# Kernel tuning notes

Measured on AMD Instinct MI355X. Metric: run time of the kernel, lower is better.

The kernel has to match this reference:

```python
import jax, jax.numpy as jnp
import numpy as np

N, F_IN, HID, H1, NG = 50000, 128, 64, 4, 512
E = 800000


def setup_inputs() -> dict:
    key = jax.random.key(0)
    ks = jax.random.split(key, 16)
    x = jax.random.normal(ks[0], (N, F_IN), dtype=jnp.float32)
    edge_index = jax.random.randint(ks[1], (2, E), 0, N, dtype=jnp.int64)
    batch = jnp.sort(jax.random.randint(ks[2], (N,), 0, NG, dtype=jnp.int64))
    s = 0.05
    W1 = jax.random.normal(ks[3], (F_IN, H1 * HID), dtype=jnp.float32) * s
    a_src1 = jax.random.normal(ks[4], (H1, HID), dtype=jnp.float32) * s
    a_dst1 = jax.random.normal(ks[5], (H1, HID), dtype=jnp.float32) * s
    b1 = jnp.zeros((H1 * HID,), dtype=jnp.float32)
    W2 = jax.random.normal(ks[6], (H1 * HID, HID), dtype=jnp.float32) * s
    a_src2 = jax.random.normal(ks[7], (1, HID), dtype=jnp.float32) * s
    a_dst2 = jax.random.normal(ks[8], (1, HID), dtype=jnp.float32) * s
    b2 = jnp.zeros((HID,), dtype=jnp.float32)
    Wc = jax.random.normal(ks[9], (HID, 2), dtype=jnp.float32) * s
    bc = jnp.zeros((2,), dtype=jnp.float32)
    return dict(x=x, edge_index=edge_index, batch=batch, W1=W1, a_src1=a_src1,
                a_dst1=a_dst1, b1=b1, W2=W2, a_src2=a_src2, a_dst2=a_dst2,
                b2=b2, Wc=Wc, bc=bc)


def gat_layer(x, W, a_src, a_dst, bias, src, dst, n):
    # PyG GATConv: h = x @ W per head; e_ij = LeakyReLU(a_src.h_j + a_dst.h_i),
    # softmax over incoming edges of each dst node, then scatter-add aggregate.
    H, D = a_src.shape
    h = (x @ W).reshape(n, H, D)                       # [N,H,D]
    asrc = jnp.einsum('nhd,hd->nh', h, a_src)          # [N,H]
    adst = jnp.einsum('nhd,hd->nh', h, a_dst)
    e = jax.nn.leaky_relu(asrc[src] + adst[dst], 0.2)  # [E,H]
    m = jax.lax.stop_gradient(jax.ops.segment_max(e, dst, num_segments=n))
    p = jnp.exp(e - m[dst])
    s = jax.ops.segment_sum(p, dst, num_segments=n)
    alpha = p / (s[dst] + 1e-16)                       # [E,H]
    out = jax.ops.segment_sum(alpha[:, :, None] * h[src], dst, num_segments=n)
    return out.reshape(n, H * D) + bias


def reference(x, edge_index, batch, W1, a_src1, a_dst1, b1, W2, a_src2, a_dst2, b2, Wc, bc):
    n = x.shape[0]
    loops = jnp.arange(n, dtype=edge_index.dtype)
    src = jnp.concatenate([edge_index[0], loops])  # add self-loops (PyG default)
    dst = jnp.concatenate([edge_index[1], loops])
    h = jax.nn.relu(gat_layer(x, W1, a_src1, a_dst1, b1, src, dst, n))
    h = jax.nn.relu(gat_layer(h, W2, a_src2, a_dst2, b2, src, dst, n))
    # global mean pool over graphs
    ng = NG
    sums = jax.ops.segment_sum(h, batch, num_segments=ng)
    cnts = jax.ops.segment_sum(jnp.ones((n,), h.dtype), batch, num_segments=ng)
    pooled = sums / jnp.maximum(cnts, 1.0)[:, None]
    logits = pooled @ Wc + bc
    return jax.nn.log_softmax(logits, axis=1)
```

## Files before the change

kernel.cpp:

```cpp
#include <hip/hip_runtime.h>
#include <hip/hip_bf16.h>
#include <cstddef>
#include <cstdint>

#define FIN   128
#define HID   64
#define H1    4
#define NGRAPH 512
#define BCAP  8192
#define PREB  512

typedef short bf16x8 __attribute__((ext_vector_type(8)));
typedef float f32x4  __attribute__((ext_vector_type(4)));

#if defined(__has_builtin)
#if __has_builtin(__builtin_amdgcn_cvt_f32_fp8) && __has_builtin(__builtin_amdgcn_cvt_pk_fp8_f32)
#define HAVE_HW_FP8 1
#endif
#endif

__device__ __forceinline__ float wave_reduce_sum(float v) {
  #pragma unroll
  for (int off = 32; off > 0; off >>= 1) v += __shfl_down(v, off, 64);
  return v;
}

__device__ __forceinline__ float leaky02(float x) {
  return x > 0.0f ? x : 0.2f * x;
}

__device__ __forceinline__ unsigned short f2bf(float f) {
  union { float f; unsigned int i; } v; v.f = f;
  unsigned int b = v.i;
  return (unsigned short)((b + 0x7FFFu + ((b >> 16) & 1u)) >> 16);
}

#ifndef HAVE_HW_FP8
__device__ __forceinline__ unsigned char f2fp8_1(float f) {
  unsigned int u = __float_as_uint(f);
  unsigned int s = u >> 31;
  u &= 0x7fffffffu;
  if (u > 0x43e00000u) u = 0x43e00000u;
  unsigned int b = u + (0x0007FFFFu + ((u >> 20) & 1u));
  int e = (int)(b >> 23) - 127;
  unsigned int m = (b >> 20) & 7u;
  unsigned char o;
  if (e < -9) o = 0;
  else if (e < -6) { int sh = -6 - e; o = (unsigned char)((8u | m) >> sh); }
  else if (e > 8) o = 0x7e;
  else o = (unsigned char)(((e + 7) << 3) | m);
  return o | (unsigned char)(s << 7);
}
__device__ __forceinline__ float fp8tof_1(unsigned char b) {
  unsigned int s = b >> 7, e = (b >> 3) & 15u, m = b & 7u;
  float v = (e == 0) ? (float)m * 0.001953125f
                     : (float)(8u + m) * __uint_as_float((117u + e) << 23);
  return s ? -v : v;
}
#endif

__device__ __forceinline__ unsigned char f2fp8(float f) {
#ifdef HAVE_HW_FP8
  return (unsigned char)(__builtin_amdgcn_cvt_pk_fp8_f32(f, f, 0u, false) & 0xffu);
#else
  return f2fp8_1(f);
#endif
}
__device__ __forceinline__ float fp8dec(unsigned int w, int i) {
#ifdef HAVE_HW_FP8
  switch (i) {
    case 0: return __builtin_amdgcn_cvt_f32_fp8(w, 0);
    case 1: return __builtin_amdgcn_cvt_f32_fp8(w, 1);
    case 2: return __builtin_amdgcn_cvt_f32_fp8(w, 2);
    default: return __builtin_amdgcn_cvt_f32_fp8(w, 3);
  }
#else
  return fp8tof_1((unsigned char)((w >> (8 * i)) & 0xffu));
#endif
}

__global__ __launch_bounds__(256)
void pre_kernel(const float* __restrict__ W1, const float* __restrict__ W2,
                unsigned short* __restrict__ W1T, unsigned short* __restrict__ W2T,
                const int* __restrict__ dst, int* __restrict__ bucketCnt,
                const int* __restrict__ batch, int* __restrict__ gstart,
                int* __restrict__ gend, int E, int N, int nbuck) {
  __shared__ int lh[256];
  int tid = threadIdx.x;
  lh[tid] = 0;
  __syncthreads();
  int stride = gridDim.x * 256;
  int t0 = blockIdx.x * 256 + tid;
  for (int i = t0; i < E; i += stride)
    atomicAdd(&lh[dst[i] >> 8], 1);
  for (int i = t0; i < N; i += stride) {
    int g = batch[i];
    if (i == 0 || batch[i - 1] != g) gstart[g] = i;
    if (i == N - 1 || batch[i + 1] != g) gend[g] = i + 1;
  }
  for (int u = t0; u < 256 * 128; u += stride) {
    int n = u >> 7, k = u & 127;
    W1T[u] = f2bf(W1[(size_t)k * 256 + n]);
  }
  for (int u = t0; u < 64 * 256; u += stride) {
    int n = u >> 8, k = u & 255;
    W2T[u] = f2bf(W2[(size_t)k * 64 + n]);
  }
  __syncthreads();
  if (tid < nbuck && lh[tid] > 0) atomicAdd(&bucketCnt[tid], lh[tid]);
}

#define P3K 16
__global__ __launch_bounds__(256)
void bpart_kernel(const int* __restrict__ src, const int* __restrict__ dst,
                  int* __restrict__ bucketFill, unsigned int* __restrict__ bucketBuf,
                  int E, int nbuck) {
  __shared__ int lhist[256];
  __shared__ int lbase[256];
  int tid = threadIdx.x;
  int chunk = 256 * P3K;
  for (int start = blockIdx.x * chunk; start < E; start += gridDim.x * chunk) {
    lhist[tid] = 0;
    __syncthreads();
    int mybuck[P3K]; unsigned int mypack[P3K]; int myrank[P3K];
    #pragma unroll
    for (int k = 0; k < P3K; k++) {
      int i = start + k * 256 + tid;
      if (i < E) {
        int d = dst[i];
        int b = d >> 8;
        mybuck[k] = b;
        mypack[k] = (unsigned int)src[i] | ((unsigned int)(d & 255) << 16);
        myrank[k] = atomicAdd(&lhist[b], 1);
      } else mybuck[k] = -1;
    }
    __syncthreads();
    if (tid < nbuck) lbase[tid] = (lhist[tid] > 0) ? atomicAdd(&bucketFill[tid], lhist[tid]) : 0;
    __syncthreads();
    #pragma unroll
    for (int k = 0; k < P3K; k++) {
      if (mybuck[k] >= 0) {
        int b = mybuck[k];
        int pos = lbase[b] + myrank[k];
        if (pos < BCAP) bucketBuf[((size_t)b << 13) + pos] = mypack[k];
      }
    }
    __syncthreads();
  }
}

__global__ __launch_bounds__(256)
void bbuild_kernel(const unsigned int* __restrict__ bucketBuf, const int* __restrict__ bucketCnt,
                   int* __restrict__ rowstart, int* __restrict__ rowend,
                   unsigned short* __restrict__ csr, int N) {
  __shared__ int ldeg[256];
  __shared__ int lscan[256];
  __shared__ int lfill[256];
  int b = blockIdx.x;
  int tid = threadIdx.x;
  int r0 = b << 13;
  int cnt = bucketCnt[b]; if (cnt > BCAP) cnt = BCAP;
  int nb0 = b << 8;
  ldeg[tid] = 0;
  __syncthreads();
  for (int j = tid; j < cnt; j += 256)
    atomicAdd(&ldeg[bucketBuf[r0 + j] >> 16], 1);
  __syncthreads();
  int v = ldeg[tid];
  lscan[tid] = v;
  __syncthreads();
  for (int off = 1; off < 256; off <<= 1) {
    int u = (tid >= off) ? lscan[tid - off] : 0;
    __syncthreads();
    lscan[tid] += u;
    __syncthreads();
  }
  int excl = lscan[tid] - v;
  lfill[tid] = excl;
  if (nb0 + tid < N) {
    rowstart[nb0 + tid] = r0 + excl;
    rowend[nb0 + tid]   = r0 + excl + v;
  }
  __syncthreads();
  for (int j = tid; j < cnt; j += 256) {
    unsigned int p = bucketBuf[r0 + j];
    int pos = r0 + atomicAdd(&lfill[p >> 16], 1);
    csr[pos] = (unsigned short)(p & 0xffffu);
  }
}

__global__ __launch_bounds__(256)
void gemm1_kernel(const float* __restrict__ X, const unsigned short* __restrict__ W1T,
                  unsigned char* __restrict__ h1f8,
                  const float* __restrict__ a_src, const float* __restrict__ a_dst,
                  float* __restrict__ asv, float* __restrict__ adv, int N) {
  __shared__ unsigned short As[64][136];
  __shared__ unsigned short Bs[256][40];
  int t = threadIdx.x;
  int w = t >> 6, lane = t & 63;
  int quad = lane >> 4, l16 = lane & 15;
  int blockRow = blockIdx.x * 64;

  {
    int node = t >> 2, kp = (t & 3) * 32;
    int gn = blockRow + node; if (gn >= N) gn = N - 1;
    const float4* xp = (const float4*)(X + (size_t)gn * 128 + kp);
    #pragma unroll
    for (int i = 0; i < 4; i++) {
      float4 va = xp[2 * i], vb = xp[2 * i + 1];
      union { unsigned short u[8]; uint4 v; } r;
      r.u[0] = f2bf(va.x); r.u[1] = f2bf(va.y); r.u[2] = f2bf(va.z); r.u[3] = f2bf(va.w);
      r.u[4] = f2bf(vb.x); r.u[5] = f2bf(vb.y); r.u[6] = f2bf(vb.z); r.u[7] = f2bf(vb.w);
      *(uint4*)&As[node][kp + i * 8] = r.v;
    }
  }

  f32x4 acc[4][4];
  #pragma unroll
  for (int i = 0; i < 4; i++)
    #pragma unroll
    for (int j = 0; j < 4; j++) acc[i][j] = (f32x4){0.f, 0.f, 0.f, 0.f};

  for (int kc = 0; kc < FIN; kc += 32) {
    {
      const unsigned short* wp = W1T + (size_t)t * 128 + kc;
      #pragma unroll
      for (int i = 0; i < 4; i++) {
        uint4 v = *(const uint4*)(wp + i * 8);
        *(uint4*)&Bs[t][i * 8] = v;
      }
    }
    __syncthreads();
    bf16x8 af[4], bfr[4];
    #pragma unroll
    for (int mt = 0; mt < 4; mt++)
      af[mt] = *(const bf16x8*)&As[mt * 16 + l16][kc + quad * 8];
    #pragma unroll
    for (int nt = 0; nt < 4; nt++)
      bfr[nt] = *(const bf16x8*)&Bs[w * 64 + nt * 16 + l16][quad * 8];
    #pragma unroll
    for (int mt = 0; mt < 4; mt++)
      #pragma unroll
      for (int nt = 0; nt < 4; nt++)
        acc[mt][nt] = __builtin_amdgcn_mfma_f32_16x16x32_bf16(af[mt], bfr[nt], acc[mt][nt], 0, 0, 0);
    __syncthreads();
  }

  float a_s[4], a_d[4];
  #pragma unroll
  for (int nt = 0; nt < 4; nt++) {
    a_s[nt] = a_src[w * 64 + nt * 16 + l16];
    a_d[nt] = a_dst[w * 64 + nt * 16 + l16];
  }
  #pragma unroll
  for (int mt = 0; mt < 4; mt++) {
    #pragma unroll
    for (int reg = 0; reg < 4; reg++) {
      int node = blockRow + mt * 16 + quad * 4 + reg;
      bool ok = node < N;
      float ps = 0.0f, pd = 0.0f;
      #pragma unroll
      for (int nt = 0; nt < 4; nt++) {
        float v = acc[mt][nt][reg];
        ps = fmaf(v, a_s[nt], ps);
        pd = fmaf(v, a_d[nt], pd);
        if (ok) h1f8[(size_t)node * 256 + w * 64 + nt * 16 + l16] = f2fp8(v);
      }
      #pragma unroll
      for (int off = 8; off > 0; off >>= 1) {
        ps += __shfl_xor(ps, off, 16);
        pd += __shfl_xor(pd, off, 16);
      }
      if (l16 == 0 && ok) {
        asv[(size_t)node * 4 + w] = ps;
        adv[(size_t)node * 4 + w] = pd;
      }
    }
  }
}

__global__ __launch_bounds__(256)
void gemm2_kernel(const unsigned short* __restrict__ out1b, const unsigned short* __restrict__ W2T,
                  unsigned char* __restrict__ h2f8,
                  const float* __restrict__ a_src, const float* __restrict__ a_dst,
                  float* __restrict__ asv, float* __restrict__ adv, int N) {
  __shared__ unsigned short As[64][40];
  __shared__ unsigned short Bs[64][40];
  int t = threadIdx.x;
  int w = t >> 6, lane = t & 63;
  int quad = lane >> 4, l16 = lane & 15;
  int blockRow = blockIdx.x * 64;

  f32x4 acc[4];
  #pragma unroll
  for (int j = 0; j < 4; j++) acc[j] = (f32x4){0.f, 0.f, 0.f, 0.f};

  int nodeS = t >> 2, koff = (t & 3) * 8;
  int gnS = blockRow + nodeS; if (gnS >= N) gnS = N - 1;

  for (int kc = 0; kc < 256; kc += 32) {
    {
      uint4 va = *(const uint4*)(out1b + (size_t)gnS * 256 + kc + koff);
      *(uint4*)&As[nodeS][koff] = va;
      uint4 vb = *(const uint4*)(W2T + (size_t)nodeS * 256 + kc + koff);
      *(uint4*)&Bs[nodeS][koff] = vb;
    }
    __syncthreads();
    bf16x8 af = *(const bf16x8*)&As[w * 16 + l16][quad * 8];
    #pragma unroll
    for (int nt = 0; nt < 4; nt++) {
      bf16x8 bfr = *(const bf16x8*)&Bs[nt * 16 + l16][quad * 8];
      acc[nt] = __builtin_amdgcn_mfma_f32_16x16x32_bf16(af, bfr, acc[nt], 0, 0, 0);
    }
    __syncthreads();
  }

  float a_s[4], a_d[4];
  #pragma unroll
  for (int nt = 0; nt < 4; nt++) {
    a_s[nt] = a_src[nt * 16 + l16];
    a_d[nt] = a_dst[nt * 16 + l16];
  }
  #pragma unroll
  for (int reg = 0; reg < 4; reg++) {
    int node = blockRow + w * 16 + quad * 4 + reg;
    bool ok = node < N;
    float ps = 0.0f, pd = 0.0f;
    #pragma unroll
    for (int nt = 0; nt < 4; nt++) {
      float v = acc[nt][reg];
      ps = fmaf(v, a_s[nt], ps);
      pd = fmaf(v, a_d[nt], pd);
      if (ok) h2f8[(size_t)node * 64 + nt * 16 + l16] = f2fp8(v);
    }
    #pragma unroll
    for (int off = 8; off > 0; off >>= 1) {
      ps += __shfl_xor(ps, off, 16);
      pd += __shfl_xor(pd, off, 16);
    }
    if (l16 == 0 && ok) { asv[node] = ps; adv[node] = pd; }
  }
}

__global__ __launch_bounds__(256)
void agg1_kernel(const unsigned char* __restrict__ h1f8, const int* __restrict__ rowstart,
                 const int* __restrict__ rowend, const unsigned short* __restrict__ csr,
                 const float* __restrict__ asv, const float* __restrict__ adv,
                 const float* __restrict__ b1, unsigned short* __restrict__ out1b, int N) {
  __shared__ int   sbuf[4][64];
  __shared__ float pbuf[4][4][68];
  int wv   = threadIdx.x >> 6;
  int lane = threadIdx.x & 63;
  int n = blockIdx.x * 4 + wv;
  if (n >= N) return;
  int r0 = rowstart[n], r1 = rowend[n];
  float4 ad = *(const float4*)(adv + (size_t)n * 4);
  float4 asn = *(const float4*)(asv + (size_t)n * 4);
  int hsel = lane >> 4;

  float es0 = leaky02(asn.x + ad.x);
  float es1 = leaky02(asn.y + ad.y);
  float es2 = leaky02(asn.z + ad.z);
  float es3 = leaky02(asn.w + ad.w);
  float esel = hsel == 0 ? es0 : (hsel == 1 ? es1 : (hsel == 2 ? es2 : es3));
  float m0r = es0, m1r = es1, m2r = es2, m3r = es3;
  float mselr = esel;
  float ssum = 0.0f;
  float a0 = 0, a1 = 0, a2 = 0, a3 = 0;

  for (int base = r0; base < r1; base += 64) {
    int j = base + lane;
    int cnt = min(64, r1 - base);
    float e0 = -1e30f, e1 = -1e30f, e2 = -1e30f, e3 = -1e30f;
    if (j < r1) {
      int s = csr[j];
      float4 as = *(const float4*)(asv + (size_t)s * 4);
      sbuf[wv][lane] = s;
      e0 = leaky02(as.x + ad.x);
      e1 = leaky02(as.y + ad.y);
      e2 = leaky02(as.z + ad.z);
      e3 = leaky02(as.w + ad.w);
    }
    float f0 = e0, f1 = e1, f2 = e2, f3 = e3;
    #pragma unroll
    for (int off = 32; off > 0; off >>= 1) {
      e0 = fmaxf(e0, __shfl_xor(e0, off, 64));
      e1 = fmaxf(e1, __shfl_xor(e1, off, 64));
      e2 = fmaxf(e2, __shfl_xor(e2, off, 64));
      e3 = fmaxf(e3, __shfl_xor(e3, off, 64));
    }
    float m0n = fmaxf(m0r, e0), m1n = fmaxf(m1r, e1);
    float m2n = fmaxf(m2r, e2), m3n = fmaxf(m3r, e3);
    float mseln = hsel == 0 ? m0n : (hsel == 1 ? m1n : (hsel == 2 ? m2n : m3n));
    float scl = __expf(mselr - mseln);
    ssum *= scl; a0 *= scl; a1 *= scl; a2 *= scl; a3 *= scl;
    m0r = m0n; m1r = m1n; m2r = m2n; m3r = m3n; mselr = mseln;

    float p0 = __expf(f0 - m0n);
    float p1 = __expf(f1 - m1n);
    float p2 = __expf(f2 - m2n);
    float p3 = __expf(f3 - m3n);
    pbuf[wv][0][lane] = p0;
    pbuf[wv][1][lane] = p1;
    pbuf[wv][2][lane] = p2;
    pbuf[wv][3][lane] = p3;
    #pragma unroll
    for (int off = 32; off > 0; off >>= 1) {
      p0 += __shfl_xor(p0, off, 64);
      p1 += __shfl_xor(p1, off, 64);
      p2 += __shfl_xor(p2, off, 64);
      p3 += __shfl_xor(p3, off, 64);
    }
    ssum += hsel == 0 ? p0 : (hsel == 1 ? p1 : (hsel == 2 ? p2 : p3));
    __threadfence_block();

    int c = 0;
    for (; c + 4 <= cnt; c += 4) {
      int4 sv = *(const int4*)&sbuf[wv][c];
      int sc0 = __builtin_amdgcn_readfirstlane(sv.x);
      int sc1 = __builtin_amdgcn_readfirstlane(sv.y);
      int sc2 = __builtin_amdgcn_readfirstlane(sv.z);
      int sc3 = __builtin_amdgcn_readfirstlane(sv.w);
      unsigned int hw0 = *((const unsigned int*)(h1f8 + ((size_t)sc0 << 8)) + lane);
      unsigned int hw1 = *((const unsigned int*)(h1f8 + ((size_t)sc1 << 8)) + lane);
      unsigned int hw2 = *((const unsigned int*)(h1f8 + ((size_t)sc2 << 8)) + lane);
      unsigned int hw3 = *((const unsigned int*)(h1f8 + ((size_t)sc3 << 8)) + lane);
      float4 pv = *(const float4*)&pbuf[wv][hsel][c];
      a0 = fmaf(pv.x, fp8dec(hw0, 0), a0);
      a1 = fmaf(pv.x, fp8dec(hw0, 1), a1);
      a2 = fmaf(pv.x, fp8dec(hw0, 2), a2);
      a3 = fmaf(pv.x, fp8dec(hw0, 3), a3);
      a0 = fmaf(pv.y, fp8dec(hw1, 0), a0);
      a1 = fmaf(pv.y, fp8dec(hw1, 1), a1);
      a2 = fmaf(pv.y, fp8dec(hw1, 2), a2);
      a3 = fmaf(pv.y, fp8dec(hw1, 3), a3);
      a0 = fmaf(pv.z, fp8dec(hw2, 0), a0);
      a1 = fmaf(pv.z, fp8dec(hw2, 1), a1);
      a2 = fmaf(pv.z, fp8dec(hw2, 2), a2);
      a3 = fmaf(pv.z, fp8dec(hw2, 3), a3);
      a0 = fmaf(pv.w, fp8dec(hw3, 0), a0);
      a1 = fmaf(pv.w, fp8dec(hw3, 1), a1);
      a2 = fmaf(pv.w, fp8dec(hw3, 2), a2);
      a3 = fmaf(pv.w, fp8dec(hw3, 3), a3);
    }
    for (; c < cnt; c++) {
      int sc = __builtin_amdgcn_readfirstlane(sbuf[wv][c]);
      float psel = pbuf[wv][hsel][c];
      unsigned int hw = *((const unsigned int*)(h1f8 + ((size_t)sc << 8)) + lane);
      a0 = fmaf(psel, fp8dec(hw, 0), a0);
      a1 = fmaf(psel, fp8dec(hw, 1), a1);
      a2 = fmaf(psel, fp8dec(hw, 2), a2);
      a3 = fmaf(psel, fp8dec(hw, 3), a3);
    }
    __threadfence_block();
  }

  {
    float psel = __expf(esel - mselr);
    ssum += psel;
    unsigned int hw = *((const unsigned int*)(h1f8 + ((size_t)n << 8)) + lane);
    a0 = fmaf(psel, fp8dec(hw, 0), a0);
    a1 = fmaf(psel, fp8dec(hw, 1), a1);
    a2 = fmaf(psel, fp8dec(hw, 2), a2);
    a3 = fmaf(psel, fp8dec(hw, 3), a3);
  }

  float inv = 1.0f / (ssum + 1e-16f);
  int d0 = lane * 4;
  float4 bv = *(const float4*)(b1 + d0);
  float v0 = a0 * inv + bv.x;
  float v1 = a1 * inv + bv.y;
  float v2 = a2 * inv + bv.z;
  float v3 = a3 * inv + bv.w;
  ushort4 o;
  o.x = f2bf(v0 > 0 ? v0 : 0.0f);
  o.y = f2bf(v1 > 0 ? v1 : 0.0f);
  o.z = f2bf(v2 > 0 ? v2 : 0.0f);
  o.w = f2bf(v3 > 0 ? v3 : 0.0f);
  *(ushort4*)(out1b + (size_t)n * 256 + d0) = o;
}

__global__ __launch_bounds__(256)
void agg2_kernel(const unsigned char* __restrict__ h2f8, const int* __restrict__ rowstart,
                 const int* __restrict__ rowend, const unsigned short* __restrict__ csr,
                 const float* __restrict__ asv, const float* __restrict__ adv,
                 const float* __restrict__ b2, float* __restrict__ h2out, int N) {
  __shared__ int   sbuf[4][64];
  __shared__ float pbuf[4][64];
  int wv   = threadIdx.x >> 6;
  int lane = threadIdx.x & 63;
  int quad = lane >> 4, l16 = lane & 15;
  int n = blockIdx.x * 4 + wv;
  if (n >= N) return;
  int r0 = rowstart[n], r1 = rowend[n];
  float ad = adv[n];
  float eself = leaky02(asv[n] + ad);
  float m = eself;
  float ssum = 0.0f;
  float a0 = 0, a1 = 0, a2 = 0, a3 = 0;

  for (int base = r0; base < r1; base += 64) {
    int j = base + lane;
    int cnt = min(64, r1 - base);
    float e = -1e30f;
    if (j < r1) {
      int s = csr[j];
      sbuf[wv][lane] = s;
      e = leaky02(asv[s] + ad);
    }
    float f = e;
    #pragma unroll
    for (int off = 32; off > 0; off >>= 1)
      e = fmaxf(e, __shfl_xor(e, off, 64));
    float mnew = fmaxf(m, e);
    float scl = __expf(m - mnew);
    ssum *= scl; a0 *= scl; a1 *= scl; a2 *= scl; a3 *= scl;
    m = mnew;

    float p = __expf(f - mnew);
    pbuf[wv][lane] = p;
    #pragma unroll
    for (int off = 32; off > 0; off >>= 1)
      p += __shfl_xor(p, off, 64);
    ssum += p;
    __threadfence_block();

    int c = 0;
    for (; c + 8 <= cnt; c += 8) {
      int scA = sbuf[wv][c + quad];
      int scB = sbuf[wv][c + 4 + quad];
      float pA = pbuf[wv][c + quad];
      float pB = pbuf[wv][c + 4 + quad];
      unsigned int hwA = *((const unsigned int*)(h2f8 + ((size_t)scA << 6)) + l16);
      unsigned int hwB = *((const unsigned int*)(h2f8 + ((size_t)scB << 6)) + l16);
      a0 = fmaf(pA, fp8dec(hwA, 0), a0);
      a1 = fmaf(pA, fp8dec(hwA, 1), a1);
      a2 = fmaf(pA, fp8dec(hwA, 2), a2);
      a3 = fmaf(pA, fp8dec(hwA, 3), a3);
      a0 = fmaf(pB, fp8dec(hwB, 0), a0);
      a1 = fmaf(pB, fp8dec(hwB, 1), a1);
      a2 = fmaf(pB, fp8dec(hwB, 2), a2);
      a3 = fmaf(pB, fp8dec(hwB, 3), a3);
    }
    for (; c + 4 <= cnt; c += 4) {
      int sc = sbuf[wv][c + quad];
      float p1 = pbuf[wv][c + quad];
      unsigned int hw = *((const unsigned int*)(h2f8 + ((size_t)sc << 6)) + l16);
      a0 = fmaf(p1, fp8dec(hw, 0), a0);
      a1 = fmaf(p1, fp8dec(hw, 1), a1);
      a2 = fmaf(p1, fp8dec(hw, 2), a2);
      a3 = fmaf(p1, fp8dec(hw, 3), a3);
    }
    int rem = cnt - c;
    if (quad < rem) {
      int sc = sbuf[wv][c + quad];
      float p1 = pbuf[wv][c + quad];
      unsigned int hw = *((const unsigned int*)(h2f8 + ((size_t)sc << 6)) + l16);
      a0 = fmaf(p1, fp8dec(hw, 0), a0);
      a1 = fmaf(p1, fp8dec(hw, 1), a1);
      a2 = fmaf(p1, fp8dec(hw, 2), a2);
      a3 = fmaf(p1, fp8dec(hw, 3), a3);
    }
    __threadfence_block();
  }

  #pragma unroll
  for (int off = 16; off <= 32; off <<= 1) {
    a0 += __shfl_xor(a0, off, 64);
    a1 += __shfl_xor(a1, off, 64);
    a2 += __shfl_xor(a2, off, 64);
    a3 += __shfl_xor(a3, off, 64);
  }

  {
    float p = __expf(eself - m);
    ssum += p;
    unsigned int hw = *((const unsigned int*)(h2f8 + ((size_t)n << 6)) + l16);
    a0 = fmaf(p, fp8dec(hw, 0), a0);
    a1 = fmaf(p, fp8dec(hw, 1), a1);
    a2 = fmaf(p, fp8dec(hw, 2), a2);
    a3 = fmaf(p, fp8dec(hw, 3), a3);
  }

  if (quad == 0) {
    float inv = 1.0f / (ssum + 1e-16f);
    float4 bv = *(const float4*)(b2 + l16 * 4);
    float4 o;
    float v0 = a0 * inv + bv.x;
    float v1 = a1 * inv + bv.y;
    float v2 = a2 * inv + bv.z;
    float v3 = a3 * inv + bv.w;
    o.x = v0 > 0 ? v0 : 0.0f;
    o.y = v1 > 0 ? v1 : 0.0f;
    o.z = v2 > 0 ? v2 : 0.0f;
    o.w = v3 > 0 ? v3 : 0.0f;
    *(float4*)(h2out + (size_t)n * 64 + l16 * 4) = o;
  }
}

__global__ __launch_bounds__(256)
void pool_kernel(const float* __restrict__ h2, const int* __restrict__ gstart,
                 const int* __restrict__ gend, const float* __restrict__ Wc,
                 const float* __restrict__ bc, float* __restrict__ out) {
  int g = blockIdx.x;
  int w = threadIdx.x >> 6, lane = threadIdx.x & 63;
  int s = gstart[g], e = gend[g];
  float acc = 0.0f;
  for (int n = s + w; n < e; n += 4) acc += h2[(size_t)n * 64 + lane];
  __shared__ float red[4][64];
  red[w][lane] = acc;
  __syncthreads();
  if (w == 0) {
    float v = red[0][lane] + red[1][lane] + red[2][lane] + red[3][lane];
    float pooled = (e > s) ? v / (float)(e - s) : 0.0f;
    float l0 = wave_reduce_sum(pooled * Wc[lane * 2 + 0]);
    float l1 = wave_reduce_sum(pooled * Wc[lane * 2 + 1]);
    if (lane == 0) {
      l0 += bc[0]; l1 += bc[1];
      float mx = fmaxf(l0, l1);
      float lse = mx + logf(__expf(l0 - mx) + __expf(l1 - mx));
      out[g * 2 + 0] = l0 - lse;
      out[g * 2 + 1] = l1 - lse;
    }
  }
}

extern "C" void kernel_launch(void* const* d_in, const int* in_sizes, int n_in,
                              void* d_out, int out_size, void* d_ws, size_t ws_size,
                              hipStream_t stream) {
  const float* x      = (const float*)d_in[0];
  const int*   ei     = (const int*)d_in[1];
  const int*   batch  = (const int*)d_in[2];
  const float* W1     = (const float*)d_in[3];
  const float* a_src1 = (const float*)d_in[4];
  const float* a_dst1 = (const float*)d_in[5];
  const float* b1     = (const float*)d_in[6];
  const float* W2     = (const float*)d_in[7];
  const float* a_src2 = (const float*)d_in[8];
  const float* a_dst2 = (const float*)d_in[9];
  const float* b2     = (const float*)d_in[10];
  const float* Wc     = (const float*)d_in[11];
  const float* bc     = (const float*)d_in[12];
  float* out = (float*)d_out;

  const int N = in_sizes[0] / FIN;
  const int E = in_sizes[1] / 2;
  const int* srcArr = ei;
  const int* dstArr = ei + E;
  const int nbuck = (N + 255) >> 8;

  char* base = (char*)d_ws;
  size_t off = 0;
  auto alloc = [&](size_t bytes) -> void* {
    void* p = base + off;
    off = (off + bytes + 255) & ~(size_t)255;
    return p;
  };
  unsigned short* W1T  = (unsigned short*)alloc((size_t)256 * 128 * 2);
  unsigned short* W2T  = (unsigned short*)alloc((size_t)64 * 256 * 2);
  unsigned char*  h1f8 = (unsigned char*)alloc((size_t)N * 256);
  unsigned short* out1b= (unsigned short*)alloc((size_t)N * 256 * 2);
  unsigned char*  h2f8 = (unsigned char*)alloc((size_t)N * 64);
  float* h2    = (float*)alloc((size_t)N * 64 * 4);
  float* asv1  = (float*)alloc((size_t)N * 4 * 4);
  float* adv1  = (float*)alloc((size_t)N * 4 * 4);
  float* asv2  = (float*)alloc((size_t)N * 4);
  float* adv2  = (float*)alloc((size_t)N * 4);
  int*   bucketCnt = (int*)alloc(256 * 4);
  int*   bucketFill= (int*)alloc(256 * 4);
  int*   gstart= (int*)alloc(NGRAPH * 4);
  int*   gend  = (int*)alloc(NGRAPH * 4);
  size_t zspan = (size_t)((char*)gend + NGRAPH * 4 - (char*)bucketCnt);
  int*   rowstart = (int*)alloc((size_t)N * 4);
  int*   rowend   = (int*)alloc((size_t)N * 4);
  unsigned int* bucketBuf = (unsigned int*)alloc((size_t)nbuck * BCAP * 4);
  unsigned short* csr = (unsigned short*)alloc((size_t)nbuck * BCAP * 2);
  (void)ws_size; (void)n_in; (void)out_size;

  int gridWv = (N + 3) / 4;
  int gridG  = (N + 63) / 64;
  int gridP3 = (E + 256 * P3K - 1) / (256 * P3K);

  hipMemsetAsync(bucketCnt, 0, zspan, stream);
  pre_kernel<<<PREB, 256, 0, stream>>>(W1, W2, W1T, W2T, dstArr, bucketCnt,
                                       batch, gstart, gend, E, N, nbuck);
  bpart_kernel<<<gridP3, 256, 0, stream>>>(srcArr, dstArr, bucketFill, bucketBuf, E, nbuck);
  bbuild_kernel<<<nbuck, 256, 0, stream>>>(bucketBuf, bucketCnt, rowstart, rowend, csr, N);

  gemm1_kernel<<<gridG, 256, 0, stream>>>(x, W1T, h1f8, a_src1, a_dst1, asv1, adv1, N);
  agg1_kernel<<<gridWv, 256, 0, stream>>>(h1f8, rowstart, rowend, csr, asv1, adv1, b1, out1b, N);

  gemm2_kernel<<<gridG, 256, 0, stream>>>(out1b, W2T, h2f8, a_src2, a_dst2, asv2, adv2, N);
  agg2_kernel<<<gridWv, 256, 0, stream>>>(h2f8, rowstart, rowend, csr, asv2, adv2, b2, h2, N);

  pool_kernel<<<NGRAPH, 256, 0, stream>>>(h2, gstart, gend, Wc, bc, out);
}
```

Baseline: 246.2 us.

## Replace online softmax max with global per-head upper bound from GEMM epilogue

New measurement: 307.3 us. 1.25x slower.

```diff
diff --git a/kernel.cpp b/kernel.cpp
--- a/kernel.cpp
+++ b/kernel.cpp
@@ -33,6 +33,15 @@
   union { float f; unsigned int i; } v; v.f = f;
   unsigned int b = v.i;
   return (unsigned short)((b + 0x7FFFu + ((b >> 16) & 1u)) >> 16);
+}
+
+__device__ __forceinline__ unsigned int fkey(float f) {
+  unsigned int b = __float_as_uint(f);
+  return (b & 0x80000000u) ? ~b : (b | 0x80000000u);
+}
+__device__ __forceinline__ float funkey(unsigned int k) {
+  unsigned int b = (k & 0x80000000u) ? (k ^ 0x80000000u) : ~k;
+  return __uint_as_float(b);
 }
 
 #ifndef HAVE_HW_FP8
@@ -193,7 +202,8 @@
 void gemm1_kernel(const float* __restrict__ X, const unsigned short* __restrict__ W1T,
                   unsigned char* __restrict__ h1f8,
                   const float* __restrict__ a_src, const float* __restrict__ a_dst,
-                  float* __restrict__ asv, float* __restrict__ adv, int N) {
+                  float* __restrict__ asv, float* __restrict__ adv,
+                  unsigned int* __restrict__ maxk1, int N) {
   __shared__ unsigned short As[64][136];
   __shared__ unsigned short Bs[256][40];
   int t = threadIdx.x;
@@ -252,6 +262,7 @@
     a_s[nt] = a_src[w * 64 + nt * 16 + l16];
     a_d[nt] = a_dst[w * 64 + nt * 16 + l16];
   }
+  float wmax = -1e30f;
   #pragma unroll
   for (int mt = 0; mt < 4; mt++) {
     #pragma unroll
@@ -271,19 +282,24 @@
         ps += __shfl_xor(ps, off, 16);
         pd += __shfl_xor(pd, off, 16);
       }
+      if (ok) wmax = fmaxf(wmax, ps);
       if (l16 == 0 && ok) {
         asv[(size_t)node * 4 + w] = ps;
         adv[(size_t)node * 4 + w] = pd;
       }
     }
   }
+  wmax = fmaxf(wmax, __shfl_xor(wmax, 16, 64));
+  wmax = fmaxf(wmax, __shfl_xor(wmax, 32, 64));
+  if (lane == 0) atomicMax(&maxk1[w], fkey(wmax));
 }
 
 __global__ __launch_bounds__(256)
 void gemm2_kernel(const unsigned short* __restrict__ out1b, const unsigned short* __restrict__ W2T,
                   unsigned char* __restrict__ h2f8,
                   const float* __restrict__ a_src, const float* __restrict__ a_dst,
-                  float* __restrict__ asv, float* __restrict__ adv, int N) {
+                  float* __restrict__ asv, float* __restrict__ adv,
+                  unsigned int* __restrict__ maxk2, int N) {
   __shared__ unsigned short As[64][40];
   __shared__ unsigned short Bs[64][40];
   int t = threadIdx.x;
@@ -321,6 +337,7 @@
     a_s[nt] = a_src[nt * 16 + l16];
     a_d[nt] = a_dst[nt * 16 + l16];
   }
+  float wmax = -1e30f;
   #pragma unroll
   for (int reg = 0; reg < 4; reg++) {
     int node = blockRow + w * 16 + quad * 4 + reg;
@@ -338,14 +355,19 @@
       ps += __shfl_xor(ps, off, 16);
       pd += __shfl_xor(pd, off, 16);
     }
+    if (ok) wmax = fmaxf(wmax, ps);
     if (l16 == 0 && ok) { asv[node] = ps; adv[node] = pd; }
   }
+  wmax = fmaxf(wmax, __shfl_xor(wmax, 16, 64));
+  wmax = fmaxf(wmax, __shfl_xor(wmax, 32, 64));
+  if (lane == 0) atomicMax(&maxk2[0], fkey(wmax));
 }
 
 __global__ __launch_bounds__(256)
 void agg1_kernel(const unsigned char* __restrict__ h1f8, const int* __restrict__ rowstart,
                  const int* __restrict__ rowend, const unsigned short* __restrict__ csr,
                  const float* __restrict__ asv, const float* __restrict__ adv,
+                 const unsigned int* __restrict__ maxk1,
                  const float* __restrict__ b1, unsigned short* __restrict__ out1b, int N) {
   __shared__ int   sbuf[4][64];
   __shared__ float pbuf[4][4][68];
@@ -358,60 +380,37 @@
   float4 asn = *(const float4*)(asv + (size_t)n * 4);
   int hsel = lane >> 4;
 
+  float m0 = leaky02(funkey(maxk1[0]) + ad.x);
+  float m1 = leaky02(funkey(maxk1[1]) + ad.y);
+  float m2 = leaky02(funkey(maxk1[2]) + ad.z);
+  float m3 = leaky02(funkey(maxk1[3]) + ad.w);
+  float msel = hsel == 0 ? m0 : (hsel == 1 ? m1 : (hsel == 2 ? m2 : m3));
   float es0 = leaky02(asn.x + ad.x);
   float es1 = leaky02(asn.y + ad.y);
   float es2 = leaky02(asn.z + ad.z);
   float es3 = leaky02(asn.w + ad.w);
   float esel = hsel == 0 ? es0 : (hsel == 1 ? es1 : (hsel == 2 ? es2 : es3));
-  float m0r = es0, m1r = es1, m2r = es2, m3r = es3;
-  float mselr = esel;
-  float ssum = 0.0f;
+
+  float q0 = 0, q1 = 0, q2 = 0, q3 = 0;
   float a0 = 0, a1 = 0, a2 = 0, a3 = 0;
 
   for (int base = r0; base < r1; base += 64) {
     int j = base + lane;
     int cnt = min(64, r1 - base);
-    float e0 = -1e30f, e1 = -1e30f, e2 = -1e30f, e3 = -1e30f;
     if (j < r1) {
       int s = csr[j];
       float4 as = *(const float4*)(asv + (size_t)s * 4);
       sbuf[wv][lane] = s;
-      e0 = leaky02(as.x + ad.x);
-      e1 = leaky02(as.y + ad.y);
-      e2 = leaky02(as.z + ad.z);
-      e3 = leaky02(as.w + ad.w);
-    }
-    float f0 = e0, f1 = e1, f2 = e2, f3 = e3;
-    #pragma unroll
-    for (int off = 32; off > 0; off >>= 1) {
-      e0 = fmaxf(e0, __shfl_xor(e0, off, 64));
-      e1 = fmaxf(e1, __shfl_xor(e1, off, 64));
-      e2 = fmaxf(e2, __shfl_xor(e2, off, 64));
-      e3 = fmaxf(e3, __shfl_xor(e3, off, 64));
-    }
-    float m0n = fmaxf(m0r, e0), m1n = fmaxf(m1r, e1);
-    float m2n = fmaxf(m2r, e2), m3n = fmaxf(m3r, e3);
-    float mseln = hsel == 0 ? m0n : (hsel == 1 ? m1n : (hsel == 2 ? m2n : m3n));
-    float scl = __expf(mselr - mseln);
-    ssum *= scl; a0 *= scl; a1 *= scl; a2 *= scl; a3 *= scl;
-    m0r = m0n; m1r = m1n; m2r = m2n; m3r = m3n; mselr = mseln;
-
-    float p0 = __expf(f0 - m0n);
-    float p1 = __expf(f1 - m1n);
-    float p2 = __expf(f2 - m2n);
-    float p3 = __expf(f3 - m3n);
-    pbuf[wv][0][lane] = p0;
-    pbuf[wv][1][lane] = p1;
-    pbuf[wv][2][lane] = p2;
-    pbuf[wv][3][lane] = p3;
-    #pragma unroll
-    for (int off = 32; off > 0; off >>= 1) {
-      p0 += __shfl_xor(p0, off, 64);
-      p1 += __shfl_xor(p1, off, 64);
-      p2 += __shfl_xor(p2, off, 64);
-      p3 += __shfl_xor(p3, off, 64);
-    }
-    ssum += hsel == 0 ? p0 : (hsel == 1 ? p1 : (hsel == 2 ? p2 : p3));
+      float p0 = __expf(leaky02(as.x + ad.x) - m0);
+      float p1 = __expf(leaky02(as.y + ad.y) - m1);
+      float p2 = __expf(leaky02(as.z + ad.z) - m2);
+      float p3 = __expf(leaky02(as.w + ad.w) - m3);
+      pbuf[wv][0][lane] = p0;
+      pbuf[wv][1][lane] = p1;
+      pbuf[wv][2][lane] = p2;
+      pbuf[wv][3][lane] = p3;
+      q0 += p0; q1 += p1; q2 += p2; q3 += p3;
+    }
     __threadfence_block();
 
     int c = 0;
@@ -455,8 +454,17 @@
     __threadfence_block();
   }
 
+  #pragma unroll
+  for (int off = 32; off > 0; off >>= 1) {
+    q0 += __shfl_xor(q0, off, 64);
+    q1 += __shfl_xor(q1, off, 64);
+    q2 += __shfl_xor(q2, off, 64);
+    q3 += __shfl_xor(q3, off, 64);
+  }
+  float ssum = hsel == 0 ? q0 : (hsel == 1 ? q1 : (hsel == 2 ? q2 : q3));
+
   {
-    float psel = __expf(esel - mselr);
+    float psel = __expf(esel - msel);
     ssum += psel;
     unsigned int hw = *((const unsigned int*)(h1f8 + ((size_t)n << 8)) + lane);
     a0 = fmaf(psel, fp8dec(hw, 0), a0);
@@ -484,6 +492,7 @@
 void agg2_kernel(const unsigned char* __restrict__ h2f8, const int* __restrict__ rowstart,
                  const int* __restrict__ rowend, const unsigned short* __restrict__ csr,
                  const float* __restrict__ asv, const float* __restrict__ adv,
+                 const unsigned int* __restrict__ maxk2,
                  const float* __restrict__ b2, float* __restrict__ h2out, int N) {
   __shared__ int   sbuf[4][64];
   __shared__ float pbuf[4][64];
@@ -494,35 +503,21 @@
   if (n >= N) return;
   int r0 = rowstart[n], r1 = rowend[n];
   float ad = adv[n];
+  float m = leaky02(funkey(maxk2[0]) + ad);
   float eself = leaky02(asv[n] + ad);
-  float m = eself;
-  float ssum = 0.0f;
+  float q = 0.0f;
   float a0 = 0, a1 = 0, a2 = 0, a3 = 0;
 
   for (int base = r0; base < r1; base += 64) {
     int j = base + lane;
     int cnt = min(64, r1 - base);
-    float e = -1e30f;
     if (j < r1) {
       int s = csr[j];
       sbuf[wv][lane] = s;
-      e = leaky02(asv[s] + ad);
-    }
-    float f = e;
-    #pragma unroll
-    for (int off = 32; off > 0; off >>= 1)
-      e = fmaxf(e, __shfl_xor(e, off, 64));
-    float mnew = fmaxf(m, e);
-    float scl = __expf(m - mnew);
-    ssum *= scl; a0 *= scl; a1 *= scl; a2 *= scl; a3 *= scl;
-    m = mnew;
-
-    float p = __expf(f - mnew);
-    pbuf[wv][lane] = p;
-    #pragma unroll
-    for (int off = 32; off > 0; off >>= 1)
-      p += __shfl_xor(p, off, 64);
-    ssum += p;
+      float p = __expf(leaky02(asv[s] + ad) - m);
+      pbuf[wv][lane] = p;
+      q += p;
+    }
     __threadfence_block();
 
     int c = 0;
@@ -565,12 +560,15 @@
   }
 
   #pragma unroll
+  for (int off = 32; off > 0; off >>= 1) q += __shfl_xor(q, off, 64);
+  #pragma unroll
   for (int off = 16; off <= 32; off <<= 1) {
     a0 += __shfl_xor(a0, off, 64);
     a1 += __shfl_xor(a1, off, 64);
     a2 += __shfl_xor(a2, off, 64);
     a3 += __shfl_xor(a3, off, 64);
   }
+  float ssum = q;
 
   {
     float p = __expf(eself - m);
@@ -670,7 +668,8 @@
   int*   bucketFill= (int*)alloc(256 * 4);
   int*   gstart= (int*)alloc(NGRAPH * 4);
   int*   gend  = (int*)alloc(NGRAPH * 4);
-  size_t zspan = (size_t)((char*)gend + NGRAPH * 4 - (char*)bucketCnt);
+  unsigned int* maxk = (unsigned int*)alloc(8 * 4);
+  size_t zspan = (size_t)((char*)maxk + 8 * 4 - (char*)bucketCnt);
   int*   rowstart = (int*)alloc((size_t)N * 4);
   int*   rowend   = (int*)alloc((size_t)N * 4);
   unsigned int* bucketBuf = (unsigned int*)alloc((size_t)nbuck * BCAP * 4);
@@ -687,11 +686,11 @@
   bpart_kernel<<<gridP3, 256, 0, stream>>>(srcArr, dstArr, bucketFill, bucketBuf, E, nbuck);
   bbuild_kernel<<<nbuck, 256, 0, stream>>>(bucketBuf, bucketCnt, rowstart, rowend, csr, N);
 
-  gemm1_kernel<<<gridG, 256, 0, stream>>>(x, W1T, h1f8, a_src1, a_dst1, asv1, adv1, N);
-  agg1_kernel<<<gridWv, 256, 0, stream>>>(h1f8, rowstart, rowend, csr, asv1, adv1, b1, out1b, N);
-
-  gemm2_kernel<<<gridG, 256, 0, stream>>>(out1b, W2T, h2f8, a_src2, a_dst2, asv2, adv2, N);
-  agg2_kernel<<<gridWv, 256, 0, stream>>>(h2f8, rowstart, rowend, csr, asv2, adv2, b2, h2, N);
+  gemm1_kernel<<<gridG, 256, 0, stream>>>(x, W1T, h1f8, a_src1, a_dst1, asv1, adv1, maxk, N);
+  agg1_kernel<<<gridWv, 256, 0, stream>>>(h1f8, rowstart, rowend, csr, asv1, adv1, maxk, b1, out1b, N);
+
+  gemm2_kernel<<<gridG, 256, 0, stream>>>(out1b, W2T, h2f8, a_src2, a_dst2, asv2, adv2, maxk + 4, N);
+  agg2_kernel<<<gridWv, 256, 0, stream>>>(h2f8, rowstart, rowend, csr, asv2, adv2, maxk + 4, b2, h2, N);
 
   pool_kernel<<<NGRAPH, 256, 0, stream>>>(h2, gstart, gend, Wc, bc, out);
 }
```
